# Optimization experiments

Hardware: AMD Instinct MI355X
Metric: run time of the kernel (lower is better)

## Reference

```python
import jax, jax.numpy as jnp
import numpy as np

EPS = 1e-8
N_REFINE = 10
LR_REFINE = 0.1
N_SAMPLES = 12
M_BLEND = 0.3      # self.m
MARGIN = 0.2
TAU = 0.07
USE_INFONCE = True


def safe_norm(x, axis=-1):
    return x / jnp.clip(jnp.linalg.norm(x, axis=axis, keepdims=True), EPS, None)


def setup_inputs() -> dict:
    key = jax.random.key(0)
    k1, k2, k3, k4 = jax.random.split(key, 4)
    K, C, N, H, W = 10, 768, 8, 64, 64
    fg_proto = safe_norm(jax.random.normal(k1, (K, C), jnp.float32))
    bg_proto = safe_norm(jax.random.normal(k2, (K, C), jnp.float32))
    F_map = jax.random.normal(k3, (N, C, H, W), jnp.float32)
    M_map = jax.random.uniform(k4, (N, 1, H, W), jnp.float32)
    return {"fg_proto": fg_proto, "bg_proto": bg_proto, "F_map": F_map, "M_map": M_map}


def _refine(feats, p0):
    """Iterative spherical k-means style refinement.
    feats: [S, C] unit vectors (constants), p0: [K, C] centers.
    Vectorized segment-sum version of the per-cluster torch loop
    (updates within one iteration are independent across k)."""
    K = p0.shape[0]
    ones = jnp.ones((feats.shape[0],), feats.dtype)

    def body(p, it):
        step = LR_REFINE / (1.0 + 0.5 * it)
        assign = jnp.argmax(feats @ p.T, axis=1)                      # [S]
        sums = jax.ops.segment_sum(feats, assign, num_segments=K)    # [K, C]
        cnts = jax.ops.segment_sum(ones, assign, num_segments=K)     # [K]
        mean = sums / jnp.clip(cnts, 1.0, None)[:, None]
        new = safe_norm((1.0 - step) * p + step * mean)
        p = jnp.where((cnts > 0)[:, None], new, p)
        return p, None

    p, _ = jax.lax.scan(body, p0, jnp.arange(N_REFINE, dtype=p0.dtype))
    return p


def reference(fg_proto, bg_proto, F_map, M_map):
    N, C, H, W = F_map.shape
    # mask already at feature resolution -> nearest interpolate is identity
    M_flat = jnp.clip(M_map, 0.0, 1.0).reshape(-1)                   # [N*H*W]
    F_flat = safe_norm(jnp.transpose(F_map, (0, 2, 3, 1)).reshape(-1, C))

    # min cosine distance to any prototype == 1 - max similarity
    dist_fg_min = 1.0 - jnp.max(F_flat @ fg_proto.T, axis=1)
    dist_bg_min = 1.0 - jnp.max(F_flat @ bg_proto.T, axis=1)
    score_fg = jax.lax.stop_gradient(dist_fg_min * M_flat)
    score_bg = jax.lax.stop_gradient(dist_bg_min * (1.0 - M_flat))
    pos_idx = jax.lax.top_k(score_fg, N_SAMPLES)[1]
    neg_idx = jax.lax.top_k(score_bg, N_SAMPLES)[1]

    pos_feats = F_flat[pos_idx]                                       # [12, C]
    neg_feats = F_flat[neg_idx]

    # refinement runs under torch.no_grad on detached copies
    p_fg = _refine(jax.lax.stop_gradient(pos_feats), jax.lax.stop_gradient(fg_proto))
    p_bg = _refine(jax.lax.stop_gradient(neg_feats), jax.lax.stop_gradient(bg_proto))

    # triplet loss
    pos_n = safe_norm(pos_feats)
    neg_n = safe_norm(neg_feats)
    sim_pos = jnp.mean(jnp.max(pos_n @ p_fg.T, axis=1))
    sim_neg = jnp.mean(jnp.max(neg_n @ p_fg.T, axis=1))
    loss = jax.nn.relu(MARGIN + sim_neg - sim_pos)

    if USE_INFONCE:
        pos_sim = pos_n @ p_fg.T / TAU                                # [12, K]
        neg_sim = pos_n @ p_bg.T / TAU                                # [12, K]
        numer = jax.nn.logsumexp(pos_sim, axis=1)
        denom = jax.nn.logsumexp(jnp.concatenate([pos_sim, neg_sim], axis=1), axis=1)
        loss = loss + 0.25 * (-jnp.mean(numer - denom))

    refined_fg = safe_norm((1.0 - M_BLEND) * fg_proto + M_BLEND * p_fg)
    refined_bg = safe_norm((1.0 - M_BLEND) * bg_proto + M_BLEND * p_bg)
    return loss, refined_fg, refined_bg
```

## Files before the change

kernel.cpp:

```cpp
#include <hip/hip_runtime.h>
#include <math.h>

#define KP   10
#define CC   768
#define NB   8
#define HW   4096
#define STOT 32768
#define NS   12
#define NBLK 256
#define NREG 8

#define WS_CAND  0
#define WS_FEATS 12352
#define WS_PFG   30784
#define WS_PBG   38464

typedef unsigned long long ull;
typedef float f2v __attribute__((ext_vector_type(2)));

__device__ __forceinline__ f2v fma2(f2v a, float b, f2v c) {
#if __has_builtin(__builtin_elementwise_fma)
    f2v bb = b;
    return __builtin_elementwise_fma(a, bb, c);
#else
    f2v r; r.x = fmaf(a.x, b, c.x); r.y = fmaf(a.y, b, c.y); return r;
#endif
}

__device__ __forceinline__ float dpp_sum64(float x) {
#define DPP_ADD(ctrl) \
    x += __uint_as_float((unsigned)__builtin_amdgcn_update_dpp(0, (int)__float_as_uint(x), ctrl, 0xf, 0xf, true))
    DPP_ADD(0x111);
    DPP_ADD(0x112);
    DPP_ADD(0x114);
    DPP_ADD(0x118);
    DPP_ADD(0x142);
    DPP_ADD(0x143);
#undef DPP_ADD
    return x;
}
__device__ __forceinline__ float bcast63(float x) {
    return __uint_as_float((unsigned)__builtin_amdgcn_readlane((int)__float_as_uint(x), 63));
}

__device__ __forceinline__ ull pack_key(float v, int idx) {
    unsigned u = __float_as_uint(v);
    u ^= (unsigned)((int)u >> 31) | 0x80000000u;
    return ((ull)u << 32) | (ull)(0xFFFFFFFFu - (unsigned)idx);
}

__global__ __launch_bounds__(1024) void k_scores(const float* __restrict__ fg,
                                                 const float* __restrict__ bg,
                                                 const float* __restrict__ F,
                                                 const float* __restrict__ M,
                                                 ull* __restrict__ cand) {
    __shared__ float pl[20 * CC];
    __shared__ float part[8][64][2][21];
    __shared__ ull kfl[128], kbl[128];

    const int tid  = threadIdx.x;
    const int w    = __builtin_amdgcn_readfirstlane(tid >> 6);
    const int lane = tid & 63;
    const int b    = blockIdx.x;
    const int n    = b >> 5;
    const int hwb  = (b & 31) * 128 + lane * 2;
    const float* fp = F + ((size_t)n * CC) * HW + hwb;
    const int cbase = w * 48;

    f2v fnA[8], fnB[8];
#pragma unroll
    for (int j = 0; j < 8; ++j)
        fnA[j] = __builtin_nontemporal_load((const f2v*)(fp + (size_t)(cbase + j) * HW));
#pragma unroll
    for (int j = 0; j < 8; ++j)
        fnB[j] = __builtin_nontemporal_load((const f2v*)(fp + (size_t)(cbase + 8 + j) * HW));

    for (int i = tid; i < KP * CC; i += 1024) {
        pl[i]           = fg[i];
        pl[KP * CC + i] = bg[i];
    }
    __syncthreads();

    f2v afg[KP], abg[KP], n2;
#pragma unroll
    for (int k = 0; k < KP; ++k) { afg[k] = 0.f; abg[k] = 0.f; }
    n2 = 0.f;

    for (int c0 = 0; c0 < 48; c0 += 8) {
        f2v f[8];
#pragma unroll
        for (int j = 0; j < 8; ++j) { f[j] = fnA[j]; fnA[j] = fnB[j]; }
        if (c0 + 16 < 48) {
#pragma unroll
            for (int j = 0; j < 8; ++j)
                fnB[j] = __builtin_nontemporal_load((const f2v*)(fp + (size_t)(cbase + c0 + 16 + j) * HW));
        }

#pragma unroll
        for (int k = 0; k < KP; ++k) {
            const float4* pq = (const float4*)&pl[k * CC + cbase + c0];
            float4 a = pq[0], c = pq[1];
            f2v acc = afg[k];
            acc = fma2(f[0], a.x, acc); acc = fma2(f[1], a.y, acc);
            acc = fma2(f[2], a.z, acc); acc = fma2(f[3], a.w, acc);
            acc = fma2(f[4], c.x, acc); acc = fma2(f[5], c.y, acc);
            acc = fma2(f[6], c.z, acc); acc = fma2(f[7], c.w, acc);
            afg[k] = acc;
        }
#pragma unroll
        for (int k = 0; k < KP; ++k) {
            const float4* pq = (const float4*)&pl[(KP + k) * CC + cbase + c0];
            float4 a = pq[0], c = pq[1];
            f2v acc = abg[k];
            acc = fma2(f[0], a.x, acc); acc = fma2(f[1], a.y, acc);
            acc = fma2(f[2], a.z, acc); acc = fma2(f[3], a.w, acc);
            acc = fma2(f[4], c.x, acc); acc = fma2(f[5], c.y, acc);
            acc = fma2(f[6], c.z, acc); acc = fma2(f[7], c.w, acc);
            abg[k] = acc;
        }
#pragma unroll
        for (int j = 0; j < 8; ++j) {
#if __has_builtin(__builtin_elementwise_fma)
            n2 = __builtin_elementwise_fma(f[j], f[j], n2);
#else
            n2.x = fmaf(f[j].x, f[j].x, n2.x); n2.y = fmaf(f[j].y, f[j].y, n2.y);
#endif
        }
    }

    if (w >= 8) {
#pragma unroll
        for (int k = 0; k < KP; ++k) {
            part[w - 8][lane][0][k]      = afg[k].x; part[w - 8][lane][1][k]      = afg[k].y;
            part[w - 8][lane][0][10 + k] = abg[k].x; part[w - 8][lane][1][10 + k] = abg[k].y;
        }
        part[w - 8][lane][0][20] = n2.x; part[w - 8][lane][1][20] = n2.y;
    }
    __syncthreads();
    if (w < 8) {
#pragma unroll
        for (int k = 0; k < KP; ++k) {
            part[w][lane][0][k]      += afg[k].x; part[w][lane][1][k]      += afg[k].y;
            part[w][lane][0][10 + k] += abg[k].x; part[w][lane][1][10 + k] += abg[k].y;
        }
        part[w][lane][0][20] += n2.x; part[w][lane][1][20] += n2.y;
    }
    __syncthreads();

    if (tid < 128) {
        const int lane2 = tid >> 1, j = tid & 1;
        float vals[21];
#pragma unroll
        for (int q = 0; q < 21; ++q) {
            float acc = 0.f;
#pragma unroll
            for (int ss = 0; ss < 8; ++ss) acc += part[ss][lane2][j][q];
            vals[q] = acc;
        }
        float mfg = vals[0], mbg = vals[10];
#pragma unroll
        for (int k = 1; k < KP; ++k) { mfg = fmaxf(mfg, vals[k]); mbg = fmaxf(mbg, vals[10 + k]); }
        float nc = fmaxf(sqrtf(vals[20]), 1e-8f);
        int sp = b * 128 + tid;
        float m = fminf(fmaxf(M[sp], 0.f), 1.f);
        kfl[tid] = pack_key((1.f - mfg / nc) * m, sp);
        kbl[tid] = pack_key((1.f - mbg / nc) * (1.f - m), sp);
    }
    __syncthreads();

    if (w == 0) {
        ull k0 = kfl[lane], k1 = kfl[64 + lane];
        for (int r = 0; r < NS; ++r) {
            ull bk = (k0 > k1) ? k0 : k1;
#pragma unroll
            for (int m2 = 1; m2 < 64; m2 <<= 1) {
                ull o = __shfl_xor(bk, m2, 64);
                bk = (o > bk) ? o : bk;
            }
            if (lane == 0) cand[b * NS + r] = bk;
            if (k0 == bk) k0 = 0ull;
            if (k1 == bk) k1 = 0ull;
        }
    } else if (w == 1) {
        ull k0 = kbl[lane], k1 = kbl[64 + lane];
        for (int r = 0; r < NS; ++r) {
            ull bk = (k0 > k1) ? k0 : k1;
#pragma unroll
            for (int m2 = 1; m2 < 64; m2 <<= 1) {
                ull o = __shfl_xor(bk, m2, 64);
                bk = (o > bk) ? o : bk;
            }
            if (lane == 0) cand[NBLK * NS + b * NS + r] = bk;
            if (k0 == bk) k0 = 0ull;
            if (k1 == bk) k1 = 0ull;
        }
    }
}

__global__ __launch_bounds__(640) void k_refine_fused(const ull* __restrict__ cand,
                                                      const float* __restrict__ F,
                                                      const float* __restrict__ fg,
                                                      const float* __restrict__ bg,
                                                      float* __restrict__ pfg,
                                                      float* __restrict__ pbg,
                                                      float* __restrict__ feats,
                                                      float* __restrict__ out) {
    __shared__ float fe[NS * CC];
    __shared__ int   seli[NS];
    __shared__ float dots[NS][KP];
    __shared__ int   assign[NS];

    const int side = blockIdx.x;
    const int tid  = threadIdx.x;
    const int wave = __builtin_amdgcn_readfirstlane(tid >> 6);
    const int lane = tid & 63;
    const int k    = wave;
    const float* p0 = (side == 0) ? fg : bg;
    float* pout     = (side == 0) ? pfg : pbg;

    if (wave == 0) {
        const ull* cs = cand + side * (NBLK * NS);
        ull tv[NS];
#pragma unroll
        for (int q = 0; q < NS; ++q) tv[q] = 0ull;
        for (int c = 0; c < 48; ++c) {
            ull key = cs[c * 64 + lane];
            if (key > tv[NS - 1]) {
#pragma unroll
                for (int q = NS - 1; q >= 1; --q) {
                    bool shift = key > tv[q - 1];
                    bool here  = !shift && (key > tv[q]);
                    tv[q] = shift ? tv[q - 1] : (here ? key : tv[q]);
                }
                if (key > tv[0]) tv[0] = key;
            }
        }
        for (int r = 0; r < NS; ++r) {
            ull bk = tv[0];
#pragma unroll
            for (int m2 = 1; m2 < 64; m2 <<= 1) {
                ull o = __shfl_xor(bk, m2, 64);
                bk = (o > bk) ? o : bk;
            }
            if (lane == 0) seli[r] = (int)(0xFFFFFFFFu - (unsigned)(bk & 0xFFFFFFFFull));
            bool win = (tv[0] == bk);
#pragma unroll
            for (int q = 0; q < NS - 1; ++q) tv[q] = win ? tv[q + 1] : tv[q];
            tv[NS - 1] = win ? 0ull : tv[NS - 1];
        }
    }
    __syncthreads();

    for (int i = tid; i < NS * CC; i += 640) {
        int srow = i / CC, c = i - srow * CC;
        int sp = seli[srow];
        int nn = sp >> 12, hh = sp & 4095;
        fe[i] = F[((size_t)nn * CC + c) * HW + hh];
    }
    __syncthreads();

    for (int row = wave; row < NS; row += KP) {
        float ssq = 0.f;
#pragma unroll
        for (int j = 0; j < 12; ++j) { float v = fe[row * CC + j * 64 + lane]; ssq = fmaf(v, v, ssq); }
        float tot = bcast63(dpp_sum64(ssq));
        float inv = 1.f / fmaxf(sqrtf(tot), 1e-8f);
#pragma unroll
        for (int j = 0; j < 12; ++j) fe[row * CC + j * 64 + lane] *= inv;
    }
    __syncthreads();

    {
        float4* fo = (float4*)(feats + side * (NS * CC));
        const float4* fi = (const float4*)fe;
        for (int i = tid; i < NS * CC / 4; i += 640) fo[i] = fi[i];
    }

    float4 fer[NREG][3];
#pragma unroll
    for (int s = 0; s < NREG; ++s)
#pragma unroll
        for (int j4 = 0; j4 < 3; ++j4)
            fer[s][j4] = *(const float4*)&fe[s * CC + j4 * 256 + lane * 4];

    float4 p[3];
#pragma unroll
    for (int j4 = 0; j4 < 3; ++j4)
        p[j4] = *(const float4*)&p0[k * CC + j4 * 256 + lane * 4];

    for (int it = 0; it < 10; ++it) {
        float step = 0.1f / (1.0f + 0.5f * (float)it);

        float d[NS];
#pragma unroll
        for (int s = 0; s < NS; ++s) d[s] = 0.f;
#pragma unroll
        for (int j4 = 0; j4 < 3; ++j4) {
            float4 pv = p[j4];
#pragma unroll
            for (int s = 0; s < NREG; ++s) {
                float4 fv = fer[s][j4];
                d[s] = fmaf(fv.x, pv.x, d[s]);
                d[s] = fmaf(fv.y, pv.y, d[s]);
                d[s] = fmaf(fv.z, pv.z, d[s]);
                d[s] = fmaf(fv.w, pv.w, d[s]);
            }
#pragma unroll
            for (int s = NREG; s < NS; ++s) {
                float4 fv = *(const float4*)&fe[s * CC + j4 * 256 + lane * 4];
                d[s] = fmaf(fv.x, pv.x, d[s]);
                d[s] = fmaf(fv.y, pv.y, d[s]);
                d[s] = fmaf(fv.z, pv.z, d[s]);
                d[s] = fmaf(fv.w, pv.w, d[s]);
            }
        }
#pragma unroll
        for (int s = 0; s < NS; ++s) d[s] = dpp_sum64(d[s]);
        if (lane == 63) {
#pragma unroll
            for (int s = 0; s < NS; ++s) dots[s][k] = d[s];
        }
        __syncthreads();

        if (tid < NS) {
            float bv = dots[tid][0]; int bk = 0;
#pragma unroll
            for (int kk = 1; kk < KP; ++kk) { float v = dots[tid][kk]; if (v > bv) { bv = v; bk = kk; } }
            assign[tid] = bk;
        }
        __syncthreads();

        int a[NS]; int cnt = 0;
#pragma unroll
        for (int s = 0; s < NS; ++s) { a[s] = assign[s]; cnt += (a[s] == k) ? 1 : 0; }

        if (cnt > 0) {
            float4 mac[3];
#pragma unroll
            for (int j4 = 0; j4 < 3; ++j4) mac[j4] = make_float4(0.f, 0.f, 0.f, 0.f);
#pragma unroll
            for (int s = 0; s < NREG; ++s) {
                if (a[s] == k) {
#pragma unroll
                    for (int j4 = 0; j4 < 3; ++j4) {
                        float4 fv = fer[s][j4];
                        mac[j4].x += fv.x; mac[j4].y += fv.y; mac[j4].z += fv.z; mac[j4].w += fv.w;
                    }
                }
            }
#pragma unroll
            for (int s = NREG; s < NS; ++s) {
                if (a[s] == k) {
#pragma unroll
                    for (int j4 = 0; j4 < 3; ++j4) {
                        float4 fv = *(const float4*)&fe[s * CC + j4 * 256 + lane * 4];
                        mac[j4].x += fv.x; mac[j4].y += fv.y; mac[j4].z += fv.z; mac[j4].w += fv.w;
                    }
                }
            }
            float fcnt = (float)cnt;
            float4 v[3]; float ss = 0.f;
#pragma unroll
            for (int j4 = 0; j4 < 3; ++j4) {
                v[j4].x = (1.0f - step) * p[j4].x + step * (mac[j4].x / fcnt);
                v[j4].y = (1.0f - step) * p[j4].y + step * (mac[j4].y / fcnt);
                v[j4].z = (1.0f - step) * p[j4].z + step * (mac[j4].z / fcnt);
                v[j4].w = (1.0f - step) * p[j4].w + step * (mac[j4].w / fcnt);
                ss = fmaf(v[j4].x, v[j4].x, ss);
                ss = fmaf(v[j4].y, v[j4].y, ss);
                ss = fmaf(v[j4].z, v[j4].z, ss);
                ss = fmaf(v[j4].w, v[j4].w, ss);
            }
            float tot = bcast63(dpp_sum64(ss));
            float inv = 1.f / fmaxf(sqrtf(tot), 1e-8f);
#pragma unroll
            for (int j4 = 0; j4 < 3; ++j4) {
                p[j4].x = v[j4].x * inv; p[j4].y = v[j4].y * inv;
                p[j4].z = v[j4].z * inv; p[j4].w = v[j4].w * inv;
            }
        }
    }

#pragma unroll
    for (int j4 = 0; j4 < 3; ++j4)
        *(float4*)&pout[k * CC + j4 * 256 + lane * 4] = p[j4];

    float4 vv[3]; float ss2 = 0.f;
#pragma unroll
    for (int j4 = 0; j4 < 3; ++j4) {
        float4 pz = *(const float4*)&p0[k * CC + j4 * 256 + lane * 4];
        vv[j4].x = 0.7f * pz.x + 0.3f * p[j4].x;
        vv[j4].y = 0.7f * pz.y + 0.3f * p[j4].y;
        vv[j4].z = 0.7f * pz.z + 0.3f * p[j4].z;
        vv[j4].w = 0.7f * pz.w + 0.3f * p[j4].w;
        ss2 = fmaf(vv[j4].x, vv[j4].x, ss2);
        ss2 = fmaf(vv[j4].y, vv[j4].y, ss2);
        ss2 = fmaf(vv[j4].z, vv[j4].z, ss2);
        ss2 = fmaf(vv[j4].w, vv[j4].w, ss2);
    }
    float tot2 = bcast63(dpp_sum64(ss2));
    float inv2 = 1.f / fmaxf(sqrtf(tot2), 1e-8f);
    float* orow = out + 1 + (side * KP + k) * CC;
#pragma unroll
    for (int j4 = 0; j4 < 3; ++j4) {
        float4 o4;
        o4.x = vv[j4].x * inv2; o4.y = vv[j4].y * inv2;
        o4.z = vv[j4].z * inv2; o4.w = vv[j4].w * inv2;
        *(float4*)&orow[j4 * 256 + lane * 4] = o4;
    }
}

__global__ __launch_bounds__(1024) void k_loss(const float* __restrict__ feats,
                                               const float* __restrict__ pfg,
                                               const float* __restrict__ pbg,
                                               float* __restrict__ out) {
    __shared__ float dots3[NS * 30];
    __shared__ float mp[NS], mn[NS], infon[NS];
    int tid = threadIdx.x, wave = tid >> 6, lane = tid & 63;

    for (int pid = wave; pid < 360; pid += 16) {
        int g = pid / 120, rr = pid % 120, s = rr / KP, k = rr % KP;
        const float4* a4 = (const float4*)(feats + ((g == 1 ? NS + s : s) * CC) + lane * 12);
        const float4* b4 = (const float4*)((g == 2 ? pbg : pfg) + k * CC + lane * 12);
        float acc = 0.f;
#pragma unroll
        for (int j = 0; j < 3; ++j) {
            float4 a = a4[j], b = b4[j];
            acc += a.x * b.x + a.y * b.y + a.z * b.z + a.w * b.w;
        }
        acc = dpp_sum64(acc);
        if (lane == 63) dots3[s * 30 + g * 10 + k] = acc;
    }
    __syncthreads();

    if (tid < NS) {
        const float* d = &dots3[tid * 30];
        float maxp = d[0], maxn = d[10];
#pragma unroll
        for (int k = 1; k < KP; ++k) { maxp = fmaxf(maxp, d[k]); maxn = fmaxf(maxn, d[10 + k]); }
        mp[tid] = maxp; mn[tid] = maxn;

        float x[KP], y[KP];
#pragma unroll
        for (int k = 0; k < KP; ++k) { x[k] = d[k] / 0.07f; y[k] = d[20 + k] / 0.07f; }
        float m10 = x[0];
#pragma unroll
        for (int k = 1; k < KP; ++k) m10 = fmaxf(m10, x[k]);
        float se = 0.f;
#pragma unroll
        for (int k = 0; k < KP; ++k) se += expf(x[k] - m10);
        float numer = logf(se) + m10;
        float m20 = m10;
#pragma unroll
        for (int k = 0; k < KP; ++k) m20 = fmaxf(m20, y[k]);
        float se2 = 0.f;
#pragma unroll
        for (int k = 0; k < KP; ++k) se2 += expf(x[k] - m20);
#pragma unroll
        for (int k = 0; k < KP; ++k) se2 += expf(y[k] - m20);
        float denom = logf(se2) + m20;
        infon[tid] = numer - denom;
    }
    __syncthreads();
    if (tid == 0) {
        float sp = 0.f, sn = 0.f, si = 0.f;
        for (int s = 0; s < NS; ++s) { sp += mp[s]; sn += mn[s]; si += infon[s]; }
        sp /= 12.f; sn /= 12.f; si /= 12.f;
        float loss = fmaxf(0.2f + sn - sp, 0.f) + 0.25f * (-si);
        out[0] = loss;
    }
}

extern "C" void kernel_launch(void* const* d_in, const int* in_sizes, int n_in,
                              void* d_out, int out_size, void* d_ws, size_t ws_size,
                              hipStream_t stream) {
    const float* fg = (const float*)d_in[0];
    const float* bg = (const float*)d_in[1];
    const float* F  = (const float*)d_in[2];
    const float* M  = (const float*)d_in[3];
    float* out = (float*)d_out;

    float* w    = (float*)d_ws;
    ull*   cand = (ull*)(w + WS_CAND);
    float* fea  = w + WS_FEATS;
    float* pfg  = w + WS_PFG;
    float* pbg  = w + WS_PBG;

    k_scores      <<<NBLK, 1024, 0, stream>>>(fg, bg, F, M, cand);
    k_refine_fused<<<2, 640, 0, stream>>>(cand, F, fg, bg, pfg, pbg, fea, out);
    k_loss        <<<1, 1024, 0, stream>>>(fea, pfg, pbg, out);
}
```

Before: 112.3 us.

## Split top-k selection and feature gather into a separate 24-block kernel

Moves the final top-12 candidate selection, the strided gather of the selected feature columns and their normalization out of the 2-block refine kernel into a new kernel with one block per selected row (24 blocks). The scattered loads with stride HW are spread across many CUs instead of being serialized in two blocks. The cost is an extra kernel launch, redundant top-k merging in every block, and a round trip through global memory for the gathered features.

```diff
diff --git a/kernel.cpp b/kernel.cpp
--- a/kernel.cpp
+++ b/kernel.cpp
@@ -197,16 +197,74 @@
     }
 }
 
-__global__ __launch_bounds__(640) void k_refine_fused(const ull* __restrict__ cand,
-                                                      const float* __restrict__ F,
-                                                      const float* __restrict__ fg,
-                                                      const float* __restrict__ bg,
-                                                      float* __restrict__ pfg,
-                                                      float* __restrict__ pbg,
-                                                      float* __restrict__ feats,
-                                                      float* __restrict__ out) {
+__global__ __launch_bounds__(256) void k_gather(const ull* __restrict__ cand,
+                                                const float* __restrict__ F,
+                                                float* __restrict__ feats) {
+    __shared__ int   sel_sh;
+    __shared__ float red[256];
+
+    const int b    = blockIdx.x;
+    const int side = b / NS, row = b - side * NS;
+    const int tid  = threadIdx.x;
+    const int wave = tid >> 6, lane = tid & 63;
+
+    if (wave == 0) {
+        const ull* cs = cand + side * (NBLK * NS);
+        ull tv[NS];
+#pragma unroll
+        for (int q = 0; q < NS; ++q) tv[q] = 0ull;
+        for (int c = 0; c < 48; ++c) {
+            ull key = cs[c * 64 + lane];
+            if (key > tv[NS - 1]) {
+#pragma unroll
+                for (int q = NS - 1; q >= 1; --q) {
+                    bool shift = key > tv[q - 1];
+                    bool here  = !shift && (key > tv[q]);
+                    tv[q] = shift ? tv[q - 1] : (here ? key : tv[q]);
+                }
+                if (key > tv[0]) tv[0] = key;
+            }
+        }
+        ull win = 0ull;
+        for (int r = 0; r <= row; ++r) {
+            ull bk = tv[0];
+#pragma unroll
+            for (int m2 = 1; m2 < 64; m2 <<= 1) {
+                ull o = __shfl_xor(bk, m2, 64);
+                bk = (o > bk) ? o : bk;
+            }
+            if (r == row) win = bk;
+            bool w0 = (tv[0] == bk);
+#pragma unroll
+            for (int q = 0; q < NS - 1; ++q) tv[q] = w0 ? tv[q + 1] : tv[q];
+            tv[NS - 1] = w0 ? 0ull : tv[NS - 1];
+        }
+        if (lane == 0) sel_sh = (int)(0xFFFFFFFFu - (unsigned)(win & 0xFFFFFFFFull));
+    }
+    __syncthreads();
+
+    const int sp = sel_sh;
+    const float* fp = F + ((size_t)(sp >> 12) * CC) * HW + (sp & 4095);
+    float v0 = fp[(size_t)(tid)       * HW];
+    float v1 = fp[(size_t)(tid + 256) * HW];
+    float v2 = fp[(size_t)(tid + 512) * HW];
+    red[tid] = v0 * v0 + v1 * v1 + v2 * v2;
+    __syncthreads();
+    for (int off = 128; off > 0; off >>= 1) { if (tid < off) red[tid] += red[tid + off]; __syncthreads(); }
+    float inv = 1.f / fmaxf(sqrtf(red[0]), 1e-8f);
+    float* fo = feats + (side * NS + row) * CC;
+    fo[tid]       = v0 * inv;
+    fo[tid + 256] = v1 * inv;
+    fo[tid + 512] = v2 * inv;
+}
+
+__global__ __launch_bounds__(640) void k_refine(const float* __restrict__ feats,
+                                                const float* __restrict__ fg,
+                                                const float* __restrict__ bg,
+                                                float* __restrict__ pfg,
+                                                float* __restrict__ pbg,
+                                                float* __restrict__ out) {
     __shared__ float fe[NS * CC];
-    __shared__ int   seli[NS];
     __shared__ float dots[NS][KP];
     __shared__ int   assign[NS];
 
@@ -218,63 +276,12 @@
     const float* p0 = (side == 0) ? fg : bg;
     float* pout     = (side == 0) ? pfg : pbg;
 
-    if (wave == 0) {
-        const ull* cs = cand + side * (NBLK * NS);
-        ull tv[NS];
-#pragma unroll
-        for (int q = 0; q < NS; ++q) tv[q] = 0ull;
-        for (int c = 0; c < 48; ++c) {
-            ull key = cs[c * 64 + lane];
-            if (key > tv[NS - 1]) {
-#pragma unroll
-                for (int q = NS - 1; q >= 1; --q) {
-                    bool shift = key > tv[q - 1];
-                    bool here  = !shift && (key > tv[q]);
-                    tv[q] = shift ? tv[q - 1] : (here ? key : tv[q]);
-                }
-                if (key > tv[0]) tv[0] = key;
-            }
-        }
-        for (int r = 0; r < NS; ++r) {
-            ull bk = tv[0];
-#pragma unroll
-            for (int m2 = 1; m2 < 64; m2 <<= 1) {
-                ull o = __shfl_xor(bk, m2, 64);
-                bk = (o > bk) ? o : bk;
-            }
-            if (lane == 0) seli[r] = (int)(0xFFFFFFFFu - (unsigned)(bk & 0xFFFFFFFFull));
-            bool win = (tv[0] == bk);
-#pragma unroll
-            for (int q = 0; q < NS - 1; ++q) tv[q] = win ? tv[q + 1] : tv[q];
-            tv[NS - 1] = win ? 0ull : tv[NS - 1];
-        }
-    }
-    __syncthreads();
-
-    for (int i = tid; i < NS * CC; i += 640) {
-        int srow = i / CC, c = i - srow * CC;
-        int sp = seli[srow];
-        int nn = sp >> 12, hh = sp & 4095;
-        fe[i] = F[((size_t)nn * CC + c) * HW + hh];
-    }
-    __syncthreads();
-
-    for (int row = wave; row < NS; row += KP) {
-        float ssq = 0.f;
-#pragma unroll
-        for (int j = 0; j < 12; ++j) { float v = fe[row * CC + j * 64 + lane]; ssq = fmaf(v, v, ssq); }
-        float tot = bcast63(dpp_sum64(ssq));
-        float inv = 1.f / fmaxf(sqrtf(tot), 1e-8f);
-#pragma unroll
-        for (int j = 0; j < 12; ++j) fe[row * CC + j * 64 + lane] *= inv;
-    }
-    __syncthreads();
-
     {
-        float4* fo = (float4*)(feats + side * (NS * CC));
-        const float4* fi = (const float4*)fe;
-        for (int i = tid; i < NS * CC / 4; i += 640) fo[i] = fi[i];
-    }
+        const float4* fi = (const float4*)(feats + side * (NS * CC));
+        float4* fl = (float4*)fe;
+        for (int i = tid; i < NS * CC / 4; i += 640) fl[i] = fi[i];
+    }
+    __syncthreads();
 
     float4 fer[NREG][3];
 #pragma unroll
@@ -486,7 +493,8 @@
     float* pfg  = w + WS_PFG;
     float* pbg  = w + WS_PBG;
 
-    k_scores      <<<NBLK, 1024, 0, stream>>>(fg, bg, F, M, cand);
-    k_refine_fused<<<2, 640, 0, stream>>>(cand, F, fg, bg, pfg, pbg, fea, out);
-    k_loss        <<<1, 1024, 0, stream>>>(fea, pfg, pbg, out);
-}
+    k_scores<<<NBLK, 1024, 0, stream>>>(fg, bg, F, M, cand);
+    k_gather<<<24, 256, 0, stream>>>(cand, F, fea);
+    k_refine<<<2, 640, 0, stream>>>(fea, fg, bg, pfg, pbg, out);
+    k_loss  <<<1, 1024, 0, stream>>>(fea, pfg, pbg, out);
+}
```

Measured after the change: 111.2 us. About the same (-1.0%).
